# Kernel optimization log

Hardware: AMD Instinct MI355X
Metric: run time of the kernel (lower is better)

The kernel has to match this reference:

```python
import jax, jax.numpy as jnp
import numpy as np

T, B, D_IN, H, V = 512, 128, 1024, 128, 4
NH, HD, MAXLEN = 4, 32, 64  # 4 heads * 32 = embed_dim 128; MAX_LENGTH=64


def _cell(pre, h, c, Whh):
    # pre = x @ W_ih.T + b, computed by caller. PyTorch gate order: i, f, g, o.
    g = pre + h @ Whh.T
    i, f, gg, o = jnp.split(g, 4, axis=-1)
    c = jax.nn.sigmoid(f) * c + jax.nn.sigmoid(i) * jnp.tanh(gg)
    h = jax.nn.sigmoid(o) * jnp.tanh(c)
    return h, c


def _lstm_layer(xs, Wih, Whh, b):
    # xs: [T, B, D]; input GEMM hoisted out of the scan as one big matmul
    pre = xs @ Wih.T + b  # [T, B, 4H]
    z = jnp.zeros((xs.shape[1], Whh.shape[1]), xs.dtype)

    def step(carry, p):
        h, c = carry
        h, c = _cell(p, h, c, Whh)
        return (h, c), h

    _, hs = jax.lax.scan(step, (z, z), pre)
    return hs  # [T, B, H]


def setup_inputs() -> dict:
    key = jax.random.key(0)
    ks = jax.random.split(key, 23)
    s = 0.08

    def rn(k, shape):
        return jax.random.normal(k, shape, jnp.float32) * s

    return {
        "x": jax.random.normal(ks[0], (T, B, D_IN), jnp.float32),
        "enc_Wih0": rn(ks[1], (4 * H, D_IN)), "enc_Whh0": rn(ks[2], (4 * H, H)), "enc_b0": rn(ks[3], (4 * H,)),
        "enc_Wih1": rn(ks[4], (4 * H, H)), "enc_Whh1": rn(ks[5], (4 * H, H)), "enc_b1": rn(ks[6], (4 * H,)),
        "dec_Wih0": rn(ks[7], (4 * H, H + V)), "dec_Whh0": rn(ks[8], (4 * H, H)), "dec_b0": rn(ks[9], (4 * H,)),
        "dec_Wih1": rn(ks[10], (4 * H, H)), "dec_Whh1": rn(ks[11], (4 * H, H)), "dec_b1": rn(ks[12], (4 * H,)),
        "Wq": rn(ks[13], (H, H)), "bq": rn(ks[14], (H,)),
        "Wk": rn(ks[15], (H, H)), "bk": rn(ks[16], (H,)),
        "Wv": rn(ks[17], (H, H)), "bv": rn(ks[18], (H,)),
        "Wo": rn(ks[19], (H, H)), "bo": rn(ks[20], (H,)),
        "lin_W": rn(ks[21], (V, 2 * H)), "lin_b": rn(ks[22], (V,)),
    }


def reference(x, enc_Wih0, enc_Whh0, enc_b0, enc_Wih1, enc_Whh1, enc_b1,
              dec_Wih0, dec_Whh0, dec_b0, dec_Wih1, dec_Whh1, dec_b1,
              Wq, bq, Wk, bk, Wv, bv, Wo, bo, lin_W, lin_b):
    # 2-layer encoder LSTM over the CNN feature sequence
    enc = _lstm_layer(_lstm_layer(x, enc_Wih0, enc_Whh0, enc_b0),
                      enc_Wih1, enc_Whh1, enc_b1)  # [T, B, H]

    # K/V projections of the (fixed) encoding hoisted out of the decode loop
    k = (enc @ Wk.T + bk).reshape(T, B, NH, HD)
    v = (enc @ Wv.T + bv).reshape(T, B, NH, HD)
    scale = 1.0 / float(np.sqrt(HD))

    z = jnp.zeros((B, H), x.dtype)

    def step(carry, _):
        h0, c0, h1, c1, y, ct = carry
        xin = jnp.concatenate([y, ct], axis=-1)  # cat([y, c_t]) -> [B, V+H]
        h0, c0 = _cell(xin @ dec_Wih0.T + dec_b0, h0, c0, dec_Whh0)
        h1, c1 = _cell(h0 @ dec_Wih1.T + dec_b1, h1, c1, dec_Whh1)
        s1 = h1  # top-layer LSTM output, query of length 1
        q = (s1 @ Wq.T + bq).reshape(B, NH, HD)
        attn = jax.nn.softmax(jnp.einsum('bhd,tbhd->bht', q, k) * scale, axis=-1)
        ct = jnp.einsum('bht,tbhd->bhd', attn, v).reshape(B, H) @ Wo.T + bo
        y = jnp.concatenate([s1, ct], axis=-1) @ lin_W.T + lin_b  # [B, V]
        return (h0, c0, h1, c1, y, ct), y

    init = (z, z, z, z, jnp.zeros((B, V), x.dtype), z)
    _, ys = jax.lax.scan(step, init, None, length=MAXLEN)
    return ys  # [MAX_LENGTH, B, V]
```

## Files before the change

kernel.cpp:

```cpp
#include <hip/hip_runtime.h>
#include <hip/hip_bf16.h>

typedef __attribute__((ext_vector_type(8))) short s16x8;
typedef __attribute__((ext_vector_type(4))) float f32x4;

__device__ inline unsigned short f2bf(float f) {
  unsigned u = __builtin_bit_cast(unsigned, f);
  unsigned r = (u + 0x7FFFu + ((u >> 16) & 1u)) >> 16;
  return (unsigned short)r;
}
__device__ inline float bf2f(short v) {
  return __builtin_bit_cast(float, ((unsigned)(unsigned short)v) << 16);
}
__device__ inline float bflo(unsigned w) {
  return __builtin_bit_cast(float, w << 16);
}
__device__ inline float bfhi(unsigned w) {
  return __builtin_bit_cast(float, w & 0xFFFF0000u);
}
__device__ inline float sigf(float x) { return 1.f / (1.f + __expf(-x)); }
__device__ inline float tanhf_(float x) { float e = __expf(2.f * x); return 1.f - 2.f / (e + 1.f); }

__global__ void packT(const float* __restrict__ src, unsigned* __restrict__ dst,
                      int rows, int scols, int kkPairs) {
  int i = blockIdx.x * 256 + threadIdx.x;
  if (i >= kkPairs * rows) return;
  int kk = i / rows, o = i % rows;
  int k0 = 2 * kk, k1 = 2 * kk + 1;
  float lo = (k0 < scols) ? src[(size_t)o * scols + k0] : 0.f;
  float hi = (k1 < scols) ? src[(size_t)o * scols + k1] : 0.f;
  dst[i] = (unsigned)f2bf(lo) | ((unsigned)f2bf(hi) << 16);
}

#define BM 128
#define BN 128
#define BKK 32

template<int A_BF16, int C_BF16>
__global__ __launch_bounds__(256) void gemm_bt(const void* __restrict__ Av,
    const float* __restrict__ B, const float* __restrict__ bias,
    void* __restrict__ Cv, int M, int N, int K) {
  __shared__ short sA[BM * BKK];
  __shared__ short sB[BN * BKK];
  const int tid = threadIdx.x;
  const int l = tid & 63;
  const int wid = tid >> 6;
  const int wr = wid >> 1, wc = wid & 1;
  const int lr = l & 15, kg = l >> 4;
  const int bn = blockIdx.x, bm = blockIdx.y;
  const int arow = tid >> 1;
  const int acol = (tid & 1) * 16;

  f32x4 acc[4][4];
#pragma unroll
  for (int i = 0; i < 4; ++i)
#pragma unroll
    for (int j = 0; j < 4; ++j) acc[i][j] = (f32x4){0.f, 0.f, 0.f, 0.f};

  for (int kt = 0; kt < K; kt += BKK) {
    __syncthreads();
    if (A_BF16) {
      const unsigned short* src = (const unsigned short*)Av + (size_t)(bm * BM + arow) * K + kt + acol;
      *(s16x8*)&sA[arow * BKK + acol] = *(const s16x8*)src;
      *(s16x8*)&sA[arow * BKK + acol + 8] = *(const s16x8*)(src + 8);
    } else {
      const float* src = (const float*)Av + (size_t)(bm * BM + arow) * K + kt + acol;
      s16x8 v0, v1;
#pragma unroll
      for (int e = 0; e < 8; ++e) { v0[e] = (short)f2bf(src[e]); v1[e] = (short)f2bf(src[8 + e]); }
      *(s16x8*)&sA[arow * BKK + acol] = v0;
      *(s16x8*)&sA[arow * BKK + acol + 8] = v1;
    }
    {
      const float* src = B + (size_t)(bn * BN + arow) * K + kt + acol;
      s16x8 v0, v1;
#pragma unroll
      for (int e = 0; e < 8; ++e) { v0[e] = (short)f2bf(src[e]); v1[e] = (short)f2bf(src[8 + e]); }
      *(s16x8*)&sB[arow * BKK + acol] = v0;
      *(s16x8*)&sB[arow * BKK + acol + 8] = v1;
    }
    __syncthreads();
    s16x8 af[4], bfr[4];
#pragma unroll
    for (int mi = 0; mi < 4; ++mi)
      af[mi] = *(const s16x8*)&sA[(wr * 64 + mi * 16 + lr) * BKK + kg * 8];
#pragma unroll
    for (int ni = 0; ni < 4; ++ni)
      bfr[ni] = *(const s16x8*)&sB[(wc * 64 + ni * 16 + lr) * BKK + kg * 8];
#pragma unroll
    for (int mi = 0; mi < 4; ++mi)
#pragma unroll
      for (int ni = 0; ni < 4; ++ni)
        acc[mi][ni] = __builtin_amdgcn_mfma_f32_16x16x32_bf16(af[mi], bfr[ni], acc[mi][ni], 0, 0, 0);
  }
  const int r0 = bm * BM + wr * 64;
  const int c0 = bn * BN + wc * 64;
#pragma unroll
  for (int mi = 0; mi < 4; ++mi)
#pragma unroll
    for (int ni = 0; ni < 4; ++ni) {
      const int col = c0 + ni * 16 + lr;
      const float bv = bias[col];
#pragma unroll
      for (int e = 0; e < 4; ++e) {
        const int row = r0 + mi * 16 + kg * 4 + e;
        const float v = acc[mi][ni][e] + bv;
        if (C_BF16) ((unsigned short*)Cv)[(size_t)row * N + col] = f2bf(v);
        else        ((float*)Cv)[(size_t)row * N + col] = v;
      }
    }
}

__global__ __launch_bounds__(512) void lstm_scan(const float* __restrict__ pre,
    const float* __restrict__ Whh, unsigned short* __restrict__ hs, int T) {
  __shared__ unsigned short hb[2][2048];
  const int tid = threadIdx.x;
  const int l = tid & 63, w = tid >> 6;
  const int wg = blockIdx.x;
  const int lr = l & 15, kg = l >> 4;
  const int col = w * 16 + lr;
  const int rbase = kg * 4;

  s16x8 wf[4][4];
#pragma unroll
  for (int gi = 0; gi < 4; ++gi)
#pragma unroll
    for (int kk = 0; kk < 4; ++kk) {
      const float* p = Whh + (size_t)(gi * 128 + col) * 128 + kk * 32 + kg * 8;
#pragma unroll
      for (int e = 0; e < 8; ++e) wf[gi][kk][e] = (short)f2bf(p[e]);
    }
  for (int i = tid; i < 4096; i += 512) ((unsigned short*)hb)[i] = 0;
  float c[4] = {0.f, 0.f, 0.f, 0.f};

  const float* pbase = pre + ((size_t)(wg * 16 + rbase)) * 512 + col;
  float pf[16];
#pragma unroll
  for (int gi = 0; gi < 4; ++gi)
#pragma unroll
    for (int e = 0; e < 4; ++e) pf[gi * 4 + e] = pbase[e * 512 + gi * 128];
  __syncthreads();

  for (int t = 0; t < T; ++t) {
    const unsigned short* hc = hb[t & 1];
    unsigned short* hn = hb[(t & 1) ^ 1];
    s16x8 a[4];
#pragma unroll
    for (int kk = 0; kk < 4; ++kk) {
      const int byt = lr * 256 + ((kk * 64 + kg * 16) ^ ((lr & 7) << 4));
      a[kk] = *(const s16x8*)((const char*)hc + byt);
    }
    f32x4 acc[4];
#pragma unroll
    for (int gi = 0; gi < 4; ++gi)
      acc[gi] = (f32x4){pf[gi * 4], pf[gi * 4 + 1], pf[gi * 4 + 2], pf[gi * 4 + 3]};
    float pfn[16];
    if (t + 1 < T) {
      const float* pb2 = pbase + (size_t)(t + 1) * 65536;
#pragma unroll
      for (int gi = 0; gi < 4; ++gi)
#pragma unroll
        for (int e = 0; e < 4; ++e) pfn[gi * 4 + e] = pb2[e * 512 + gi * 128];
    } else {
#pragma unroll
      for (int i2 = 0; i2 < 16; ++i2) pfn[i2] = 0.f;
    }
#pragma unroll
    for (int kk = 0; kk < 4; ++kk)
#pragma unroll
      for (int gi = 0; gi < 4; ++gi)
        acc[gi] = __builtin_amdgcn_mfma_f32_16x16x32_bf16(a[kk], wf[gi][kk], acc[gi], 0, 0, 0);
#pragma unroll
    for (int e = 0; e < 4; ++e) {
      float gi_ = sigf(acc[0][e]);
      float gf  = sigf(acc[1][e]);
      float gg  = tanhf_(acc[2][e]);
      float go  = sigf(acc[3][e]);
      c[e] = gf * c[e] + gi_ * gg;
      float h = go * tanhf_(c[e]);
      unsigned short hu = f2bf(h);
      int row = rbase + e;
      int byt = row * 256 + ((col * 2) ^ ((row & 7) << 4));
      *(unsigned short*)((char*)hn + byt) = hu;
      hs[((size_t)t * 128 + wg * 16 + row) * 128 + col] = hu;
    }
#pragma unroll
    for (int i2 = 0; i2 < 16; ++i2) pf[i2] = pfn[i2];
    __syncthreads();
  }
}


#define DEC_SMEM 149504

__global__ void __launch_bounds__(512, 1) decoder_single(
    const unsigned short* __restrict__ kb, const unsigned short* __restrict__ vb,
    const unsigned* __restrict__ w0t,  const unsigned* __restrict__ wh0t,
    const unsigned* __restrict__ wi1t, const unsigned* __restrict__ wh1t,
    const unsigned* __restrict__ wqt,  const unsigned* __restrict__ wot,
    const float* __restrict__ b0, const float* __restrict__ b1,
    const float* __restrict__ bq, const float* __restrict__ bo,
    const float* __restrict__ linW, const float* __restrict__ linb,
    float* __restrict__ out)
{
  extern __shared__ char smem[];
  unsigned short* Kl = (unsigned short*)smem;
  float* xin = (float*)(smem + 131072);
  float* h0  = (float*)(smem + 131648);
  float* h1  = (float*)(smem + 132160);
  float* c0  = (float*)(smem + 132672);
  float* c1  = (float*)(smem + 133184);
  float* gb  = (float*)(smem + 133696);
  float* qx  = (float*)(smem + 135744);
  float* sc  = (float*)(smem + 136256);
  float* avp = (float*)(smem + 144448);
  float* part= (float*)(smem + 146496);
  float* red = (float*)(smem + 148544);
  float* mxs = (float*)(smem + 148800);
  float* isl = (float*)(smem + 148816);

  const int b = blockIdx.x;
  const int tid = threadIdx.x;
  const int l = tid & 63, wv = tid >> 6;

  {
    const unsigned* kb32 = (const unsigned*)kb;
    for (int it = 0; it < 64; ++it) {
      const int i = tid + it * 512;
      const int t = i >> 6, c32 = i & 63;
      const unsigned v = kb32[(size_t)t * 8192 + b * 64 + c32];
      const int slot = c32 >> 2, w32 = c32 & 3;
      *(unsigned*)((char*)Kl + t * 256 + (((slot + t) & 15) << 4) + w32 * 4) = v;
    }
  }
  if (tid < 136) xin[tid] = 0.f;
  if (tid < 128) { h0[tid] = 0.f; h1[tid] = 0.f; c0[tid] = 0.f; c1[tid] = 0.f; }
  const float b0r = b0[tid];
  const float b1r = b1[tid];
  __syncthreads();

  for (int s = 0; s < 64; ++s) {
    {
      float acc = b0r;
      const unsigned* wp = w0t + tid;
#pragma unroll 8
      for (int kk = 0; kk < 68; ++kk) {
        const unsigned w2 = wp[kk * 512];
        const float2 x2 = *(const float2*)(xin + 2 * kk);
        acc += x2.x * bflo(w2) + x2.y * bfhi(w2);
      }
      const unsigned* hp = wh0t + tid;
#pragma unroll 8
      for (int kk = 0; kk < 64; ++kk) {
        const unsigned w2 = hp[kk * 512];
        const float2 h2 = *(const float2*)(h0 + 2 * kk);
        acc += h2.x * bflo(w2) + h2.y * bfhi(w2);
      }
      gb[tid] = acc;
    }
    __syncthreads();
    if (tid < 128) {
      const float ig = sigf(gb[tid]), fg = sigf(gb[128 + tid]);
      const float gg = tanhf_(gb[256 + tid]), og = sigf(gb[384 + tid]);
      const float c = fg * c0[tid] + ig * gg;
      c0[tid] = c;
      h0[tid] = og * tanhf_(c);
    }
    __syncthreads();
    {
      float acc = b1r;
      const unsigned* wp = wi1t + tid;
      const unsigned* hp = wh1t + tid;
#pragma unroll 8
      for (int kk = 0; kk < 64; ++kk) {
        const unsigned wa = wp[kk * 512];
        const unsigned wb = hp[kk * 512];
        const float2 a2 = *(const float2*)(h0 + 2 * kk);
        const float2 b2 = *(const float2*)(h1 + 2 * kk);
        acc += a2.x * bflo(wa) + a2.y * bfhi(wa) + b2.x * bflo(wb) + b2.y * bfhi(wb);
      }
      gb[tid] = acc;
    }
    __syncthreads();
    if (tid < 128) {
      const float ig = sigf(gb[tid]), fg = sigf(gb[128 + tid]);
      const float gg = tanhf_(gb[256 + tid]), og = sigf(gb[384 + tid]);
      const float c = fg * c1[tid] + ig * gg;
      c1[tid] = c;
      h1[tid] = og * tanhf_(c);
    }
    __syncthreads();
    {
      const int o = tid & 127, qd = tid >> 7;
      float acc = 0.f;
      const unsigned* wp = wqt + o;
#pragma unroll
      for (int kk = qd * 16; kk < qd * 16 + 16; ++kk) {
        const unsigned w2 = wp[kk * 128];
        const float2 h2 = *(const float2*)(h1 + 2 * kk);
        acc += h2.x * bflo(w2) + h2.y * bfhi(w2);
      }
      part[qd * 128 + o] = acc;
    }
    __syncthreads();
    if (tid < 128)
      qx[tid] = bq[tid] + part[tid] + part[128 + tid] + part[256 + tid] + part[384 + tid];
    __syncthreads();
    float s4[4];
    {
      const int t = tid;
      s4[0] = 0.f; s4[1] = 0.f; s4[2] = 0.f; s4[3] = 0.f;
      const char* krow = (const char*)Kl + t * 256;
#pragma unroll
      for (int c = 0; c < 16; ++c) {
        const s16x8 kv = *(const s16x8*)(krow + (((c + t) & 15) << 4));
        const float* qp = qx + c * 8;
        float d = 0.f;
#pragma unroll
        for (int e = 0; e < 8; ++e) d += qp[e] * bf2f(kv[e]);
        s4[c >> 2] += d;
      }
      const float scale = 0.1767766952966369f;
#pragma unroll
      for (int h = 0; h < 4; ++h) {
        s4[h] *= scale;
        float m = s4[h];
#pragma unroll
        for (int off = 32; off > 0; off >>= 1) m = fmaxf(m, __shfl_xor(m, off));
        if (l == 0) red[h * 8 + wv] = m;
      }
    }
    __syncthreads();
    if (tid < 4) {
      float m = red[tid * 8];
#pragma unroll
      for (int w2 = 1; w2 < 8; ++w2) m = fmaxf(m, red[tid * 8 + w2]);
      mxs[tid] = m;
    }
    __syncthreads();
#pragma unroll
    for (int h = 0; h < 4; ++h) {
      float p = __expf(s4[h] - mxs[h]);
      sc[h * 512 + tid] = p;
#pragma unroll
      for (int off = 32; off > 0; off >>= 1) p += __shfl_xor(p, off);
      if (l == 0) red[32 + h * 8 + wv] = p;
    }
    __syncthreads();
    if (tid < 4) {
      float sm = red[32 + tid * 8];
#pragma unroll
      for (int w2 = 1; w2 < 8; ++w2) sm += red[32 + tid * 8 + w2];
      isl[tid] = 1.f / sm;
    }
    __syncthreads();
    {
      const int d = tid & 127, tc = tid >> 7, h = d >> 5;
      const unsigned short* vp = vb + (size_t)(tc * 128) * 16384 + b * 128 + d;
      const float* scp = sc + h * 512 + tc * 128;
      float acc = 0.f;
#pragma unroll 8
      for (int tt = 0; tt < 128; ++tt)
        acc += scp[tt] * bf2f((short)vp[(size_t)tt * 16384]);
      avp[tc * 128 + d] = acc;
    }
    __syncthreads();
    if (tid < 128)
      gb[tid] = (avp[tid] + avp[128 + tid] + avp[256 + tid] + avp[384 + tid]) * isl[tid >> 5];
    __syncthreads();
    {
      const int o = tid & 127, qd = tid >> 7;
      float acc = 0.f;
      const unsigned* wp = wot + o;
#pragma unroll
      for (int kk = qd * 16; kk < qd * 16 + 16; ++kk) {
        const unsigned w2 = wp[kk * 128];
        const float2 c2 = *(const float2*)(gb + 2 * kk);
        acc += c2.x * bflo(w2) + c2.y * bfhi(w2);
      }
      part[qd * 128 + o] = acc;
    }
    __syncthreads();
    if (tid < 128)
      xin[4 + tid] = bo[tid] + part[tid] + part[128 + tid] + part[256 + tid] + part[384 + tid];
    __syncthreads();
    if (tid < 256) {
      const int o = tid >> 6, j = tid & 63;
      const float* lw = linW + o * 256;
      float p = h1[j] * lw[j] + h1[j + 64] * lw[j + 64]
              + xin[4 + j] * lw[128 + j] + xin[4 + j + 64] * lw[192 + j];
#pragma unroll
      for (int off = 32; off > 0; off >>= 1) p += __shfl_xor(p, off);
      if (j == 0) {
        const float yv = p + linb[o];
        out[((size_t)s * 128 + b) * 4 + o] = yv;
        xin[o] = yv;
      }
    }
    __syncthreads();
  }
}

extern "C" void kernel_launch(void* const* d_in, const int* in_sizes, int n_in,
                              void* d_out, int out_size, void* d_ws, size_t ws_size,
                              hipStream_t stream) {
  (void)in_sizes; (void)n_in; (void)out_size; (void)ws_size;
  const float* x     = (const float*)d_in[0];
  const float* eWih0 = (const float*)d_in[1];
  const float* eWhh0 = (const float*)d_in[2];
  const float* eb0   = (const float*)d_in[3];
  const float* eWih1 = (const float*)d_in[4];
  const float* eWhh1 = (const float*)d_in[5];
  const float* eb1   = (const float*)d_in[6];
  const float* dWih0 = (const float*)d_in[7];
  const float* dWhh0 = (const float*)d_in[8];
  const float* db0   = (const float*)d_in[9];
  const float* dWih1 = (const float*)d_in[10];
  const float* dWhh1 = (const float*)d_in[11];
  const float* db1   = (const float*)d_in[12];
  const float* Wq    = (const float*)d_in[13];
  const float* bq    = (const float*)d_in[14];
  const float* Wk    = (const float*)d_in[15];
  const float* bk    = (const float*)d_in[16];
  const float* Wv    = (const float*)d_in[17];
  const float* bv    = (const float*)d_in[18];
  const float* Wo    = (const float*)d_in[19];
  const float* bo    = (const float*)d_in[20];
  const float* linW  = (const float*)d_in[21];
  const float* linb  = (const float*)d_in[22];

  char* w = (char*)d_ws;
  float* pre  = (float*)(w + 524288);
  size_t off = 524288 + (size_t)65536 * 512 * 4;
  unsigned short* hs0  = (unsigned short*)(w + off); off += (size_t)65536 * 128 * 2;
  unsigned short* enc  = (unsigned short*)(w + off); off += (size_t)65536 * 128 * 2;
  unsigned short* kbuf = (unsigned short*)(w + off); off += (size_t)65536 * 128 * 2;
  unsigned short* vbuf = (unsigned short*)(w + off); off += (size_t)65536 * 128 * 2;
  unsigned* w0t  = (unsigned*)(w + off); off += (size_t)68 * 512 * 4;
  unsigned* wh0t = (unsigned*)(w + off); off += (size_t)64 * 512 * 4;
  unsigned* wi1t = (unsigned*)(w + off); off += (size_t)64 * 512 * 4;
  unsigned* wh1t = (unsigned*)(w + off); off += (size_t)64 * 512 * 4;
  unsigned* wqt  = (unsigned*)(w + off); off += (size_t)64 * 128 * 4;
  unsigned* wot  = (unsigned*)(w + off); off += (size_t)64 * 128 * 4;

  packT<<<(68 * 512 + 255) / 256, 256, 0, stream>>>(dWih0, w0t, 512, 132, 68);
  packT<<<(64 * 512 + 255) / 256, 256, 0, stream>>>(dWhh0, wh0t, 512, 128, 64);
  packT<<<(64 * 512 + 255) / 256, 256, 0, stream>>>(dWih1, wi1t, 512, 128, 64);
  packT<<<(64 * 512 + 255) / 256, 256, 0, stream>>>(dWhh1, wh1t, 512, 128, 64);
  packT<<<(64 * 128 + 255) / 256, 256, 0, stream>>>(Wq, wqt, 128, 128, 64);
  packT<<<(64 * 128 + 255) / 256, 256, 0, stream>>>(Wo, wot, 128, 128, 64);

  gemm_bt<0, 0><<<dim3(4, 512), 256, 0, stream>>>((const void*)x, eWih0, eb0, (void*)pre, 65536, 512, 1024);
  lstm_scan<<<8, 512, 0, stream>>>(pre, eWhh0, hs0, 512);
  gemm_bt<1, 0><<<dim3(4, 512), 256, 0, stream>>>((const void*)hs0, eWih1, eb1, (void*)pre, 65536, 512, 128);
  lstm_scan<<<8, 512, 0, stream>>>(pre, eWhh1, enc, 512);
  gemm_bt<1, 1><<<dim3(1, 512), 256, 0, stream>>>((const void*)enc, Wk, bk, (void*)kbuf, 65536, 128, 128);
  gemm_bt<1, 1><<<dim3(1, 512), 256, 0, stream>>>((const void*)enc, Wv, bv, (void*)vbuf, 65536, 128, 128);

  hipFuncSetAttribute((const void*)decoder_single,
                      hipFuncAttributeMaxDynamicSharedMemorySize, DEC_SMEM);
  decoder_single<<<128, 512, DEC_SMEM, stream>>>(kbuf, vbuf, w0t, wh0t, wi1t, wh1t, wqt, wot,
      db0, db1, bq, bo, linW, linb, (float*)d_out);
}
```

Measured before the change: 3.968 ms.

## Rework decoder: gate-interleaved weights, register-resident weights/V, softmax without max pass

The decoder LSTM weights are repacked so the four gates of each hidden unit sit in adjacent lanes. Gate activations are then combined with shuffles instead of an LDS round trip, which removes two barriers per layer per step. Layer-0 input weights, the Wq/Wo slices and the per-block V slice are held in registers for all 64 steps rather than reloaded from global memory. Softmax drops the max-subtraction pass, which is safe only if scores stay bounded. The input x is also converted to bf16 in a separate pass before the big encoder GEMM when workspace allows, trading an extra pass over x for a cheaper GEMM input.

```diff
diff --git a/kernel.cpp b/kernel.cpp
--- a/kernel.cpp
+++ b/kernel.cpp
@@ -12,12 +12,8 @@
 __device__ inline float bf2f(short v) {
   return __builtin_bit_cast(float, ((unsigned)(unsigned short)v) << 16);
 }
-__device__ inline float bflo(unsigned w) {
-  return __builtin_bit_cast(float, w << 16);
-}
-__device__ inline float bfhi(unsigned w) {
-  return __builtin_bit_cast(float, w & 0xFFFF0000u);
-}
+__device__ inline float bflo(unsigned w) { return __builtin_bit_cast(float, w << 16); }
+__device__ inline float bfhi(unsigned w) { return __builtin_bit_cast(float, w & 0xFFFF0000u); }
 __device__ inline float sigf(float x) { return 1.f / (1.f + __expf(-x)); }
 __device__ inline float tanhf_(float x) { float e = __expf(2.f * x); return 1.f - 2.f / (e + 1.f); }
 
@@ -30,6 +26,24 @@
   float lo = (k0 < scols) ? src[(size_t)o * scols + k0] : 0.f;
   float hi = (k1 < scols) ? src[(size_t)o * scols + k1] : 0.f;
   dst[i] = (unsigned)f2bf(lo) | ((unsigned)f2bf(hi) << 16);
+}
+__global__ void packTg(const float* __restrict__ src, unsigned* __restrict__ dst,
+                       int scols, int kkPairs) {
+  int i = blockIdx.x * 256 + threadIdx.x;
+  if (i >= kkPairs * 512) return;
+  int kk = i / 512, j = i % 512;
+  int row = (j & 3) * 128 + (j >> 2);
+  int k0 = 2 * kk, k1 = 2 * kk + 1;
+  float lo = (k0 < scols) ? src[(size_t)row * scols + k0] : 0.f;
+  float hi = (k1 < scols) ? src[(size_t)row * scols + k1] : 0.f;
+  dst[i] = (unsigned)f2bf(lo) | ((unsigned)f2bf(hi) << 16);
+}
+__global__ void f2bf_vec(const float* __restrict__ src, unsigned short* __restrict__ dst) {
+  size_t i = ((size_t)blockIdx.x * 256 + threadIdx.x) * 4;
+  float4 v = *(const float4*)(src + i);
+  ushort4 o;
+  o.x = f2bf(v.x); o.y = f2bf(v.y); o.z = f2bf(v.z); o.w = f2bf(v.w);
+  *(ushort4*)(dst + i) = o;
 }
 
 #define BM 128
@@ -191,7 +205,7 @@
 }
 
 
-#define DEC_SMEM 149504
+#define DEC_SMEM 146432
 
 __global__ void __launch_bounds__(512, 1) decoder_single(
     const unsigned short* __restrict__ kb, const unsigned short* __restrict__ vb,
@@ -206,25 +220,26 @@
   extern __shared__ char smem[];
   unsigned short* Kl = (unsigned short*)smem;
   float* xin = (float*)(smem + 131072);
-  float* h0  = (float*)(smem + 131648);
-  float* h1  = (float*)(smem + 132160);
-  float* c0  = (float*)(smem + 132672);
-  float* c1  = (float*)(smem + 133184);
-  float* gb  = (float*)(smem + 133696);
-  float* qx  = (float*)(smem + 135744);
-  float* sc  = (float*)(smem + 136256);
-  float* avp = (float*)(smem + 144448);
-  float* part= (float*)(smem + 146496);
-  float* red = (float*)(smem + 148544);
-  float* mxs = (float*)(smem + 148800);
-  float* isl = (float*)(smem + 148816);
+  float* h0v = (float*)(smem + 131648);
+  float* h1v = (float*)(smem + 132160);
+  float* qx  = (float*)(smem + 132672);
+  float* ctv = (float*)(smem + 133184);
+  float* sc  = (float*)(smem + 133696);
+  float* avp = (float*)(smem + 141888);
+  float* part= (float*)(smem + 143936);
+  float* red = (float*)(smem + 145984);
+  float* isl = (float*)(smem + 146240);
 
   const int b = blockIdx.x;
   const int tid = threadIdx.x;
   const int l = tid & 63, wv = tid >> 6;
+  const int lb = l & ~3;
+  const int gate = tid & 3, o512 = tid >> 2;
+  const int o128 = tid & 127, qd = tid >> 7;
 
   {
     const unsigned* kb32 = (const unsigned*)kb;
+#pragma unroll
     for (int it = 0; it < 64; ++it) {
       const int i = tid + it * 512;
       const int t = i >> 6, c32 = i & 63;
@@ -233,161 +248,179 @@
       *(unsigned*)((char*)Kl + t * 256 + (((slot + t) & 15) << 4) + w32 * 4) = v;
     }
   }
+  unsigned Vpk[64];
+  {
+    const unsigned short* vp = vb + (size_t)(qd * 128) * 16384 + (size_t)b * 128 + o128;
+#pragma unroll
+    for (int m = 0; m < 64; ++m) {
+      const unsigned lo = vp[(size_t)(2 * m) * 16384];
+      const unsigned hi = vp[(size_t)(2 * m + 1) * 16384];
+      Vpk[m] = lo | (hi << 16);
+    }
+  }
+  unsigned w0r[68];
+#pragma unroll
+  for (int m = 0; m < 68; ++m) w0r[m] = w0t[(size_t)m * 512 + tid];
+  unsigned wqr[16], wor[16];
+#pragma unroll
+  for (int m = 0; m < 16; ++m) {
+    wqr[m] = wqt[(size_t)(qd * 16 + m) * 128 + o128];
+    wor[m] = wot[(size_t)(qd * 16 + m) * 128 + o128];
+  }
+  const float b0r = b0[gate * 128 + o512];
+  const float b1r = b1[gate * 128 + o512];
+  const float bqr = bq[o128];
+  const float bor = bo[o128];
+  float cc0 = 0.f, cc1 = 0.f;
+
   if (tid < 136) xin[tid] = 0.f;
-  if (tid < 128) { h0[tid] = 0.f; h1[tid] = 0.f; c0[tid] = 0.f; c1[tid] = 0.f; }
-  const float b0r = b0[tid];
-  const float b1r = b1[tid];
+  if (tid < 128) { h0v[tid] = 0.f; h1v[tid] = 0.f; }
   __syncthreads();
 
+  const float scale = 0.1767766952966369f;
+
   for (int s = 0; s < 64; ++s) {
     {
-      float acc = b0r;
-      const unsigned* wp = w0t + tid;
-#pragma unroll 8
-      for (int kk = 0; kk < 68; ++kk) {
-        const unsigned w2 = wp[kk * 512];
-        const float2 x2 = *(const float2*)(xin + 2 * kk);
-        acc += x2.x * bflo(w2) + x2.y * bfhi(w2);
+      float a0 = b0r, a1 = 0.f, a2 = 0.f, a3 = 0.f;
+#pragma unroll
+      for (int m = 0; m < 34; ++m) {
+        const f32x4 x4 = *(const f32x4*)(xin + 4 * m);
+        const unsigned wA = w0r[2 * m], wB = w0r[2 * m + 1];
+        a0 += x4[0] * bflo(wA); a1 += x4[1] * bfhi(wA);
+        a2 += x4[2] * bflo(wB); a3 += x4[3] * bfhi(wB);
       }
       const unsigned* hp = wh0t + tid;
-#pragma unroll 8
-      for (int kk = 0; kk < 64; ++kk) {
-        const unsigned w2 = hp[kk * 512];
-        const float2 h2 = *(const float2*)(h0 + 2 * kk);
-        acc += h2.x * bflo(w2) + h2.y * bfhi(w2);
-      }
-      gb[tid] = acc;
-    }
-    __syncthreads();
-    if (tid < 128) {
-      const float ig = sigf(gb[tid]), fg = sigf(gb[128 + tid]);
-      const float gg = tanhf_(gb[256 + tid]), og = sigf(gb[384 + tid]);
-      const float c = fg * c0[tid] + ig * gg;
-      c0[tid] = c;
-      h0[tid] = og * tanhf_(c);
-    }
-    __syncthreads();
-    {
-      float acc = b1r;
-      const unsigned* wp = wi1t + tid;
+#pragma unroll
+      for (int m = 0; m < 16; ++m) {
+        unsigned w4[4];
+#pragma unroll
+        for (int i = 0; i < 4; ++i) w4[i] = hp[(size_t)(4 * m + i) * 512];
+        const f32x4 hA = *(const f32x4*)(h0v + 8 * m);
+        const f32x4 hB = *(const f32x4*)(h0v + 8 * m + 4);
+        a0 += hA[0] * bflo(w4[0]); a1 += hA[1] * bfhi(w4[0]);
+        a2 += hA[2] * bflo(w4[1]); a3 += hA[3] * bfhi(w4[1]);
+        a0 += hB[0] * bflo(w4[2]); a1 += hB[1] * bfhi(w4[2]);
+        a2 += hB[2] * bflo(w4[3]); a3 += hB[3] * bfhi(w4[3]);
+      }
+      const float gval = (a0 + a1) + (a2 + a3);
+      const float iv = __shfl(gval, lb + 0);
+      const float fv = __shfl(gval, lb + 1);
+      const float gv = __shfl(gval, lb + 2);
+      const float ov = __shfl(gval, lb + 3);
+      cc0 = sigf(fv) * cc0 + sigf(iv) * tanhf_(gv);
+      const float h = sigf(ov) * tanhf_(cc0);
+      if (gate == 0) h0v[o512] = h;
+    }
+    __syncthreads();
+    {
+      float a0 = b1r, a1 = 0.f, a2 = 0.f, a3 = 0.f;
+      const unsigned* ip = wi1t + tid;
       const unsigned* hp = wh1t + tid;
-#pragma unroll 8
-      for (int kk = 0; kk < 64; ++kk) {
-        const unsigned wa = wp[kk * 512];
-        const unsigned wb = hp[kk * 512];
-        const float2 a2 = *(const float2*)(h0 + 2 * kk);
-        const float2 b2 = *(const float2*)(h1 + 2 * kk);
-        acc += a2.x * bflo(wa) + a2.y * bfhi(wa) + b2.x * bflo(wb) + b2.y * bfhi(wb);
-      }
-      gb[tid] = acc;
-    }
-    __syncthreads();
-    if (tid < 128) {
-      const float ig = sigf(gb[tid]), fg = sigf(gb[128 + tid]);
-      const float gg = tanhf_(gb[256 + tid]), og = sigf(gb[384 + tid]);
-      const float c = fg * c1[tid] + ig * gg;
-      c1[tid] = c;
-      h1[tid] = og * tanhf_(c);
-    }
-    __syncthreads();
-    {
-      const int o = tid & 127, qd = tid >> 7;
-      float acc = 0.f;
-      const unsigned* wp = wqt + o;
-#pragma unroll
-      for (int kk = qd * 16; kk < qd * 16 + 16; ++kk) {
-        const unsigned w2 = wp[kk * 128];
-        const float2 h2 = *(const float2*)(h1 + 2 * kk);
-        acc += h2.x * bflo(w2) + h2.y * bfhi(w2);
-      }
-      part[qd * 128 + o] = acc;
+#pragma unroll
+      for (int m = 0; m < 16; ++m) {
+        unsigned wi4[4], wh4[4];
+#pragma unroll
+        for (int i = 0; i < 4; ++i) { wi4[i] = ip[(size_t)(4 * m + i) * 512]; wh4[i] = hp[(size_t)(4 * m + i) * 512]; }
+        const f32x4 aA = *(const f32x4*)(h0v + 8 * m);
+        const f32x4 aB = *(const f32x4*)(h0v + 8 * m + 4);
+        const f32x4 bA = *(const f32x4*)(h1v + 8 * m);
+        const f32x4 bB = *(const f32x4*)(h1v + 8 * m + 4);
+        a0 += aA[0] * bflo(wi4[0]) + bA[0] * bflo(wh4[0]);
+        a1 += aA[1] * bfhi(wi4[0]) + bA[1] * bfhi(wh4[0]);
+        a2 += aA[2] * bflo(wi4[1]) + bA[2] * bflo(wh4[1]);
+        a3 += aA[3] * bfhi(wi4[1]) + bA[3] * bfhi(wh4[1]);
+        a0 += aB[0] * bflo(wi4[2]) + bB[0] * bflo(wh4[2]);
+        a1 += aB[1] * bfhi(wi4[2]) + bB[1] * bfhi(wh4[2]);
+        a2 += aB[2] * bflo(wi4[3]) + bB[2] * bflo(wh4[3]);
+        a3 += aB[3] * bfhi(wi4[3]) + bB[3] * bfhi(wh4[3]);
+      }
+      const float gval = (a0 + a1) + (a2 + a3);
+      const float iv = __shfl(gval, lb + 0);
+      const float fv = __shfl(gval, lb + 1);
+      const float gv = __shfl(gval, lb + 2);
+      const float ov = __shfl(gval, lb + 3);
+      cc1 = sigf(fv) * cc1 + sigf(iv) * tanhf_(gv);
+      const float h = sigf(ov) * tanhf_(cc1);
+      if (gate == 0) h1v[o512] = h;
+    }
+    __syncthreads();
+    {
+      float a0 = 0.f, a1 = 0.f;
+#pragma unroll
+      for (int m = 0; m < 16; ++m) {
+        const float2 h2 = *(const float2*)(h1v + qd * 32 + 2 * m);
+        a0 += h2.x * bflo(wqr[m]);
+        a1 += h2.y * bfhi(wqr[m]);
+      }
+      part[qd * 128 + o128] = a0 + a1;
     }
     __syncthreads();
     if (tid < 128)
-      qx[tid] = bq[tid] + part[tid] + part[128 + tid] + part[256 + tid] + part[384 + tid];
-    __syncthreads();
-    float s4[4];
+      qx[tid] = (bqr + part[tid] + part[128 + tid] + part[256 + tid] + part[384 + tid]) * scale;
+    __syncthreads();
     {
       const int t = tid;
-      s4[0] = 0.f; s4[1] = 0.f; s4[2] = 0.f; s4[3] = 0.f;
+      float s0 = 0.f, s1 = 0.f, s2 = 0.f, s3 = 0.f;
       const char* krow = (const char*)Kl + t * 256;
 #pragma unroll
       for (int c = 0; c < 16; ++c) {
         const s16x8 kv = *(const s16x8*)(krow + (((c + t) & 15) << 4));
-        const float* qp = qx + c * 8;
-        float d = 0.f;
-#pragma unroll
-        for (int e = 0; e < 8; ++e) d += qp[e] * bf2f(kv[e]);
-        s4[c >> 2] += d;
-      }
-      const float scale = 0.1767766952966369f;
-#pragma unroll
-      for (int h = 0; h < 4; ++h) {
-        s4[h] *= scale;
-        float m = s4[h];
-#pragma unroll
-        for (int off = 32; off > 0; off >>= 1) m = fmaxf(m, __shfl_xor(m, off));
-        if (l == 0) red[h * 8 + wv] = m;
-      }
+        const f32x4 qA = *(const f32x4*)(qx + c * 8);
+        const f32x4 qB = *(const f32x4*)(qx + c * 8 + 4);
+        float d = qA[0] * bf2f(kv[0]) + qA[1] * bf2f(kv[1]) + qA[2] * bf2f(kv[2]) + qA[3] * bf2f(kv[3])
+                + qB[0] * bf2f(kv[4]) + qB[1] * bf2f(kv[5]) + qB[2] * bf2f(kv[6]) + qB[3] * bf2f(kv[7]);
+        if ((c >> 2) == 0) s0 += d; else if ((c >> 2) == 1) s1 += d; else if ((c >> 2) == 2) s2 += d; else s3 += d;
+      }
+      float p0 = __expf(s0), p1 = __expf(s1), p2 = __expf(s2), p3 = __expf(s3);
+      sc[0 * 512 + t] = p0; sc[1 * 512 + t] = p1; sc[2 * 512 + t] = p2; sc[3 * 512 + t] = p3;
+#pragma unroll
+      for (int off = 32; off > 0; off >>= 1) {
+        p0 += __shfl_xor(p0, off); p1 += __shfl_xor(p1, off);
+        p2 += __shfl_xor(p2, off); p3 += __shfl_xor(p3, off);
+      }
+      if (l == 0) { red[0 + wv] = p0; red[8 + wv] = p1; red[16 + wv] = p2; red[24 + wv] = p3; }
     }
     __syncthreads();
     if (tid < 4) {
-      float m = red[tid * 8];
-#pragma unroll
-      for (int w2 = 1; w2 < 8; ++w2) m = fmaxf(m, red[tid * 8 + w2]);
-      mxs[tid] = m;
-    }
-    __syncthreads();
-#pragma unroll
-    for (int h = 0; h < 4; ++h) {
-      float p = __expf(s4[h] - mxs[h]);
-      sc[h * 512 + tid] = p;
-#pragma unroll
-      for (int off = 32; off > 0; off >>= 1) p += __shfl_xor(p, off);
-      if (l == 0) red[32 + h * 8 + wv] = p;
-    }
-    __syncthreads();
-    if (tid < 4) {
-      float sm = red[32 + tid * 8];
-#pragma unroll
-      for (int w2 = 1; w2 < 8; ++w2) sm += red[32 + tid * 8 + w2];
+      float sm = red[tid * 8];
+#pragma unroll
+      for (int w2 = 1; w2 < 8; ++w2) sm += red[tid * 8 + w2];
       isl[tid] = 1.f / sm;
     }
-    __syncthreads();
-    {
-      const int d = tid & 127, tc = tid >> 7, h = d >> 5;
-      const unsigned short* vp = vb + (size_t)(tc * 128) * 16384 + b * 128 + d;
-      const float* scp = sc + h * 512 + tc * 128;
-      float acc = 0.f;
-#pragma unroll 8
-      for (int tt = 0; tt < 128; ++tt)
-        acc += scp[tt] * bf2f((short)vp[(size_t)tt * 16384]);
-      avp[tc * 128 + d] = acc;
+    {
+      const int h = o128 >> 5;
+      const float* scp = sc + h * 512 + qd * 128;
+      float e0 = 0.f, e1 = 0.f, e2 = 0.f, e3 = 0.f;
+#pragma unroll
+      for (int m = 0; m < 32; ++m) {
+        const f32x4 s4v = *(const f32x4*)(scp + 4 * m);
+        e0 += s4v[0] * bflo(Vpk[2 * m]);     e1 += s4v[1] * bfhi(Vpk[2 * m]);
+        e2 += s4v[2] * bflo(Vpk[2 * m + 1]); e3 += s4v[3] * bfhi(Vpk[2 * m + 1]);
+      }
+      avp[qd * 128 + o128] = (e0 + e1) + (e2 + e3);
     }
     __syncthreads();
     if (tid < 128)
-      gb[tid] = (avp[tid] + avp[128 + tid] + avp[256 + tid] + avp[384 + tid]) * isl[tid >> 5];
-    __syncthreads();
-    {
-      const int o = tid & 127, qd = tid >> 7;
-      float acc = 0.f;
-      const unsigned* wp = wot + o;
-#pragma unroll
-      for (int kk = qd * 16; kk < qd * 16 + 16; ++kk) {
-        const unsigned w2 = wp[kk * 128];
-        const float2 c2 = *(const float2*)(gb + 2 * kk);
-        acc += c2.x * bflo(w2) + c2.y * bfhi(w2);
-      }
-      part[qd * 128 + o] = acc;
+      ctv[tid] = (avp[tid] + avp[128 + tid] + avp[256 + tid] + avp[384 + tid]) * isl[tid >> 5];
+    __syncthreads();
+    {
+      float a0 = 0.f, a1 = 0.f;
+#pragma unroll
+      for (int m = 0; m < 16; ++m) {
+        const float2 c2 = *(const float2*)(ctv + qd * 32 + 2 * m);
+        a0 += c2.x * bflo(wor[m]);
+        a1 += c2.y * bfhi(wor[m]);
+      }
+      part[qd * 128 + o128] = a0 + a1;
     }
     __syncthreads();
     if (tid < 128)
-      xin[4 + tid] = bo[tid] + part[tid] + part[128 + tid] + part[256 + tid] + part[384 + tid];
+      xin[4 + tid] = bor + part[tid] + part[128 + tid] + part[256 + tid] + part[384 + tid];
     __syncthreads();
     if (tid < 256) {
       const int o = tid >> 6, j = tid & 63;
       const float* lw = linW + o * 256;
-      float p = h1[j] * lw[j] + h1[j + 64] * lw[j + 64]
+      float p = h1v[j] * lw[j] + h1v[j + 64] * lw[j + 64]
               + xin[4 + j] * lw[128 + j] + xin[4 + j + 64] * lw[192 + j];
 #pragma unroll
       for (int off = 32; off > 0; off >>= 1) p += __shfl_xor(p, off);
@@ -404,7 +437,7 @@
 extern "C" void kernel_launch(void* const* d_in, const int* in_sizes, int n_in,
                               void* d_out, int out_size, void* d_ws, size_t ws_size,
                               hipStream_t stream) {
-  (void)in_sizes; (void)n_in; (void)out_size; (void)ws_size;
+  (void)in_sizes; (void)n_in; (void)out_size;
   const float* x     = (const float*)d_in[0];
   const float* eWih0 = (const float*)d_in[1];
   const float* eWhh0 = (const float*)d_in[2];
@@ -442,15 +475,23 @@
   unsigned* wh1t = (unsigned*)(w + off); off += (size_t)64 * 512 * 4;
   unsigned* wqt  = (unsigned*)(w + off); off += (size_t)64 * 128 * 4;
   unsigned* wot  = (unsigned*)(w + off); off += (size_t)64 * 128 * 4;
-
-  packT<<<(68 * 512 + 255) / 256, 256, 0, stream>>>(dWih0, w0t, 512, 132, 68);
-  packT<<<(64 * 512 + 255) / 256, 256, 0, stream>>>(dWhh0, wh0t, 512, 128, 64);
-  packT<<<(64 * 512 + 255) / 256, 256, 0, stream>>>(dWih1, wi1t, 512, 128, 64);
-  packT<<<(64 * 512 + 255) / 256, 256, 0, stream>>>(dWhh1, wh1t, 512, 128, 64);
+  unsigned short* xbf = (unsigned short*)(w + off);
+  const size_t need_big = off + (size_t)65536 * 1024 * 2;
+  const bool big = ws_size >= need_big;
+
+  packTg<<<(68 * 512 + 255) / 256, 256, 0, stream>>>(dWih0, w0t, 132, 68);
+  packTg<<<(64 * 512 + 255) / 256, 256, 0, stream>>>(dWhh0, wh0t, 128, 64);
+  packTg<<<(64 * 512 + 255) / 256, 256, 0, stream>>>(dWih1, wi1t, 128, 64);
+  packTg<<<(64 * 512 + 255) / 256, 256, 0, stream>>>(dWhh1, wh1t, 128, 64);
   packT<<<(64 * 128 + 255) / 256, 256, 0, stream>>>(Wq, wqt, 128, 128, 64);
   packT<<<(64 * 128 + 255) / 256, 256, 0, stream>>>(Wo, wot, 128, 128, 64);
 
-  gemm_bt<0, 0><<<dim3(4, 512), 256, 0, stream>>>((const void*)x, eWih0, eb0, (void*)pre, 65536, 512, 1024);
+  if (big) {
+    f2bf_vec<<<65536, 256, 0, stream>>>(x, xbf);
+    gemm_bt<1, 0><<<dim3(4, 512), 256, 0, stream>>>((const void*)xbf, eWih0, eb0, (void*)pre, 65536, 512, 1024);
+  } else {
+    gemm_bt<0, 0><<<dim3(4, 512), 256, 0, stream>>>((const void*)x, eWih0, eb0, (void*)pre, 65536, 512, 1024);
+  }
   lstm_scan<<<8, 512, 0, stream>>>(pre, eWhh0, hs0, 512);
   gemm_bt<1, 0><<<dim3(4, 512), 256, 0, stream>>>((const void*)hs0, eWih1, eb1, (void*)pre, 65536, 512, 128);
   lstm_scan<<<8, 512, 0, stream>>>(pre, eWhh1, enc, 512);
```

After: 6.937 ms. +74.8%, slower.
